# Kernel optimization log

Hardware: AMD Instinct MI355X
Metric: run time of the kernel (lower is better)

The kernel has to match this reference:

```python
import jax, jax.numpy as jnp
import numpy as np


def quantize_ternary(w):
    # BitNet b1.58: scale by mean |w|, round, clamp to {-1,0,1}
    gamma = jnp.maximum(jnp.mean(jnp.abs(w)), 1e-8)
    return jnp.clip(jnp.round(w / gamma), -1.0, 1.0)


def setup_inputs() -> dict:
    key = jax.random.key(0)
    k1, k2, k3 = jax.random.split(key, 3)
    in_features, out_features = 4096, 4096
    x = jax.random.normal(k1, (4, 2048, in_features), dtype=jnp.float32)
    # kaiming_uniform-like init
    bound_w = 1.0 / np.sqrt(in_features)
    weight = jax.random.uniform(k2, (out_features, in_features), dtype=jnp.float32,
                                minval=-bound_w * np.sqrt(3.0), maxval=bound_w * np.sqrt(3.0))
    bias = jax.random.uniform(k3, (out_features,), dtype=jnp.float32,
                              minval=-bound_w, maxval=bound_w)
    return {"x": x, "weight": weight, "bias": bias}


def reference(x, weight, bias):
    qw = quantize_ternary(weight)  # [out, in], values in {-1,0,1}
    # F.linear: x @ qw.T + bias
    return jnp.einsum('bsi,oi->bso', x, qw) + bias
```

## Files before the change

kernel.cpp:

```cpp
#include <hip/hip_runtime.h>
#include <stdint.h>

#define M_DIM 8192
#define N_DIM 4096
#define K_DIM 4096
#define BM 128
#define BN 128
#define BK 64

typedef int i32x4 __attribute__((ext_vector_type(4)));
typedef float f32x4 __attribute__((ext_vector_type(4)));

__device__ __forceinline__ void async_copy16(const void* g, void* l) {
    __builtin_amdgcn_global_load_lds(
        (const __attribute__((address_space(1))) void*)g,
        (__attribute__((address_space(3))) void*)l, 16, 0, 0);
}

__global__ __launch_bounds__(256) void abssum_partial(const float4* __restrict__ w,
                                                      double* __restrict__ partials) {
    const int lane = threadIdx.x & 63;
    const int wave = threadIdx.x >> 6;
    int base = blockIdx.x * 4096 + threadIdx.x;
    float s = 0.f;
    #pragma unroll
    for (int i = 0; i < 16; i++) {
        float4 v = w[base + i * 256];
        s += fabsf(v.x) + fabsf(v.y) + fabsf(v.z) + fabsf(v.w);
    }
    double d = (double)s;
    #pragma unroll
    for (int off = 32; off > 0; off >>= 1) d += __shfl_down(d, off, 64);
    __shared__ double wsum[4];
    if (lane == 0) wsum[wave] = d;
    __syncthreads();
    if (threadIdx.x == 0)
        partials[blockIdx.x] = (wsum[0] + wsum[1]) + (wsum[2] + wsum[3]);
}

__global__ __launch_bounds__(256) void gamma_reduce(const double* __restrict__ partials,
                                                    float* __restrict__ gamma_out) {
    const int lane = threadIdx.x & 63;
    const int wave = threadIdx.x >> 6;
    double d = partials[threadIdx.x] + partials[threadIdx.x + 256] +
               partials[threadIdx.x + 512] + partials[threadIdx.x + 768];
    #pragma unroll
    for (int off = 32; off > 0; off >>= 1) d += __shfl_down(d, off, 64);
    __shared__ double wsum[4];
    if (lane == 0) wsum[wave] = d;
    __syncthreads();
    if (threadIdx.x == 0) {
        double total = (wsum[0] + wsum[1]) + (wsum[2] + wsum[3]);
        float g = (float)(total * (1.0 / 16777216.0));
        gamma_out[0] = fmaxf(g, 1e-8f);
    }
}

__global__ __launch_bounds__(256) void wquant(const float4* __restrict__ w,
                                              char4* __restrict__ qw,
                                              const float* __restrict__ gamma_p, int n4) {
    float gamma = gamma_p[0];
    int i = blockIdx.x * blockDim.x + threadIdx.x;
    if (i >= n4) return;
    float4 v = w[i];
    char4 o;
    o.x = (signed char)fminf(fmaxf(rintf(v.x / gamma), -1.f), 1.f);
    o.y = (signed char)fminf(fmaxf(rintf(v.y / gamma), -1.f), 1.f);
    o.z = (signed char)fminf(fmaxf(rintf(v.z / gamma), -1.f), 1.f);
    o.w = (signed char)fminf(fmaxf(rintf(v.w / gamma), -1.f), 1.f);
    qw[i] = o;
}

__global__ __launch_bounds__(256) void xquant(const float* __restrict__ x,
                                              char* __restrict__ xq,
                                              float* __restrict__ xscale) {
    const int row = blockIdx.x;
    const int lane = threadIdx.x & 63;
    const int wave = threadIdx.x >> 6;
    const float4* xr = (const float4*)(x + (size_t)row * K_DIM);
    float m = 0.f;
    #pragma unroll
    for (int i = 0; i < 4; i++) {
        float4 v = xr[threadIdx.x + i * 256];
        m = fmaxf(m, fmaxf(fmaxf(fabsf(v.x), fabsf(v.y)), fmaxf(fabsf(v.z), fabsf(v.w))));
    }
    #pragma unroll
    for (int off = 32; off > 0; off >>= 1) m = fmaxf(m, __shfl_down(m, off, 64));
    __shared__ float wmax[4];
    if (lane == 0) wmax[wave] = m;
    __syncthreads();
    const float mx = fmaxf(fmaxf(wmax[0], wmax[1]), fmaxf(wmax[2], wmax[3]));
    const float scale = fmaxf(mx * (1.f / 127.f), 1e-30f);
    const float inv = 1.f / scale;
    if (threadIdx.x == 0) xscale[row] = scale;
    char4* oq = (char4*)(xq + (size_t)row * K_DIM);
    #pragma unroll
    for (int i = 0; i < 4; i++) {
        float4 v = xr[threadIdx.x + i * 256];
        char4 o;
        o.x = (signed char)fminf(fmaxf(rintf(v.x * inv), -127.f), 127.f);
        o.y = (signed char)fminf(fmaxf(rintf(v.y * inv), -127.f), 127.f);
        o.z = (signed char)fminf(fmaxf(rintf(v.z * inv), -127.f), 127.f);
        o.w = (signed char)fminf(fmaxf(rintf(v.w * inv), -127.f), 127.f);
        oq[threadIdx.x + i * 256] = o;
    }
}

__global__ __launch_bounds__(256) void gemm_kernel(
    const char* __restrict__ xq,
    const char* __restrict__ qw,
    const float* __restrict__ xscale,
    const float* __restrict__ bias,
    float* __restrict__ out)
{
    __shared__ __align__(16) char As[BM * BK];
    __shared__ __align__(16) char Bs[BN * BK];

    const int tid  = threadIdx.x;
    const int wave = tid >> 6;
    const int lane = tid & 63;
    const int wm   = (wave >> 1) * 64;
    const int wn   = (wave & 1) * 64;
    const int lm   = lane & 15;
    const int quad = lane >> 4;

    const int bm = blockIdx.y * BM;
    const int bn = blockIdx.x * BN;

    const int s0    = wave * 2;
    const int srow0 = s0 * 16 + (lane >> 2);
    const int srow1 = srow0 + 16;
    const int scol  = (lane & 3) * 16;

    const char* gA0 = xq + (size_t)(bm + srow0) * K_DIM + scol;
    const char* gA1 = xq + (size_t)(bm + srow1) * K_DIM + scol;
    const char* gB0 = qw + (size_t)(bn + srow0) * K_DIM + scol;
    const char* gB1 = qw + (size_t)(bn + srow1) * K_DIM + scol;

    char* lA0 = &As[(size_t)s0 * 1024];
    char* lA1 = &As[(size_t)(s0 + 1) * 1024];
    char* lB0 = &Bs[(size_t)s0 * 1024];
    char* lB1 = &Bs[(size_t)(s0 + 1) * 1024];

    i32x4 acc[4][4];
    #pragma unroll
    for (int i = 0; i < 4; i++)
        #pragma unroll
        for (int j = 0; j < 4; j++) acc[i][j] = (i32x4){0, 0, 0, 0};

    for (int kt = 0; kt < K_DIM; kt += BK) {
        async_copy16(gA0 + kt, lA0);
        async_copy16(gA1 + kt, lA1);
        async_copy16(gB0 + kt, lB0);
        async_copy16(gB1 + kt, lB1);
        __syncthreads();

        i32x4 a[4], b[4];
        #pragma unroll
        for (int mi = 0; mi < 4; mi++)
            a[mi] = *(const i32x4*)&As[(wm + mi * 16 + lm) * BK + quad * 16];
        #pragma unroll
        for (int ni = 0; ni < 4; ni++)
            b[ni] = *(const i32x4*)&Bs[(wn + ni * 16 + lm) * BK + quad * 16];

        #pragma unroll
        for (int mi = 0; mi < 4; mi++)
            #pragma unroll
            for (int ni = 0; ni < 4; ni++)
                acc[mi][ni] = __builtin_amdgcn_mfma_i32_16x16x64_i8(
                    a[mi], b[ni], acc[mi][ni], 0, 0, 0);

        __syncthreads();
    }

    float bl[4];
    #pragma unroll
    for (int ni = 0; ni < 4; ni++) bl[ni] = bias[bn + wn + ni * 16 + lm];

    #pragma unroll
    for (int mi = 0; mi < 4; mi++) {
        #pragma unroll
        for (int r = 0; r < 4; r++) {
            const int grow = bm + wm + mi * 16 + quad * 4 + r;
            const float sc = xscale[grow];
            float* orow = out + (size_t)grow * N_DIM + bn;
            #pragma unroll
            for (int ni = 0; ni < 4; ni++)
                orow[wn + ni * 16 + lm] = sc * (float)acc[mi][ni][r] + bl[ni];
        }
    }
}

extern "C" void kernel_launch(void* const* d_in, const int* in_sizes, int n_in,
                              void* d_out, int out_size, void* d_ws, size_t ws_size,
                              hipStream_t stream) {
    const float* x    = (const float*)d_in[0];
    const float* w    = (const float*)d_in[1];
    const float* bias = (const float*)d_in[2];
    float* out = (float*)d_out;

    char* ws = (char*)d_ws;
    char*   xq       = ws;
    char*   qw       = ws + (size_t)M_DIM * K_DIM;
    float*  xscale   = (float*)(qw + (size_t)N_DIM * K_DIM);
    double* partials = (double*)(xscale + M_DIM);
    float*  gamma_p  = (float*)(partials + 1024);

    const int wn4 = (N_DIM * K_DIM) / 4;

    abssum_partial<<<1024, 256, 0, stream>>>((const float4*)w, partials);
    gamma_reduce<<<1, 256, 0, stream>>>(partials, gamma_p);
    wquant<<<(wn4 + 255) / 256, 256, 0, stream>>>((const float4*)w, (char4*)qw, gamma_p, wn4);
    xquant<<<M_DIM, 256, 0, stream>>>(x, xq, xscale);

    dim3 grid(N_DIM / BN, M_DIM / BM);
    gemm_kernel<<<grid, 256, 0, stream>>>(xq, qw, xscale, bias, out);
}
```

Baseline: 428.9 us.

## Double GEMM K-tile to 128 with XOR-swizzled LDS layout and register-cached xquant

Doubles the GEMM K tile to 128 so each sync pair covers two MFMA k-steps, halving barrier and loop overhead per unit of work. The LDS layout gains an XOR swizzle on the 16-byte chunk index, applied in both the async global-to-LDS copy and the fragment reads, to reduce bank conflicts on the wider rows. xquant now keeps its loaded float4 values in registers instead of reading x from global memory twice. Shared memory per block doubles, which may lower occupancy.

```diff
diff --git a/kernel.cpp b/kernel.cpp
--- a/kernel.cpp
+++ b/kernel.cpp
@@ -6,10 +6,9 @@
 #define K_DIM 4096
 #define BM 128
 #define BN 128
-#define BK 64
+#define BK 128
 
 typedef int i32x4 __attribute__((ext_vector_type(4)));
-typedef float f32x4 __attribute__((ext_vector_type(4)));
 
 __device__ __forceinline__ void async_copy16(const void* g, void* l) {
     __builtin_amdgcn_global_load_lds(
@@ -71,18 +70,20 @@
     qw[i] = o;
 }
 
-__global__ __launch_bounds__(256) void xquant(const float* __restrict__ x,
-                                              char* __restrict__ xq,
+__global__ __launch_bounds__(256) void xquant(const float4* __restrict__ x,
+                                              char4* __restrict__ xq,
                                               float* __restrict__ xscale) {
     const int row = blockIdx.x;
     const int lane = threadIdx.x & 63;
     const int wave = threadIdx.x >> 6;
-    const float4* xr = (const float4*)(x + (size_t)row * K_DIM);
+    const float4* xr = x + (size_t)row * (K_DIM / 4);
+    float4 v[4];
     float m = 0.f;
     #pragma unroll
     for (int i = 0; i < 4; i++) {
-        float4 v = xr[threadIdx.x + i * 256];
-        m = fmaxf(m, fmaxf(fmaxf(fabsf(v.x), fabsf(v.y)), fmaxf(fabsf(v.z), fabsf(v.w))));
+        v[i] = xr[threadIdx.x + i * 256];
+        m = fmaxf(m, fmaxf(fmaxf(fabsf(v[i].x), fabsf(v[i].y)),
+                           fmaxf(fabsf(v[i].z), fabsf(v[i].w))));
     }
     #pragma unroll
     for (int off = 32; off > 0; off >>= 1) m = fmaxf(m, __shfl_down(m, off, 64));
@@ -93,15 +94,14 @@
     const float scale = fmaxf(mx * (1.f / 127.f), 1e-30f);
     const float inv = 1.f / scale;
     if (threadIdx.x == 0) xscale[row] = scale;
-    char4* oq = (char4*)(xq + (size_t)row * K_DIM);
+    char4* oq = xq + (size_t)row * (K_DIM / 4);
     #pragma unroll
     for (int i = 0; i < 4; i++) {
-        float4 v = xr[threadIdx.x + i * 256];
         char4 o;
-        o.x = (signed char)fminf(fmaxf(rintf(v.x * inv), -127.f), 127.f);
-        o.y = (signed char)fminf(fmaxf(rintf(v.y * inv), -127.f), 127.f);
-        o.z = (signed char)fminf(fmaxf(rintf(v.z * inv), -127.f), 127.f);
-        o.w = (signed char)fminf(fmaxf(rintf(v.w * inv), -127.f), 127.f);
+        o.x = (signed char)fminf(fmaxf(rintf(v[i].x * inv), -127.f), 127.f);
+        o.y = (signed char)fminf(fmaxf(rintf(v[i].y * inv), -127.f), 127.f);
+        o.z = (signed char)fminf(fmaxf(rintf(v[i].z * inv), -127.f), 127.f);
+        o.w = (signed char)fminf(fmaxf(rintf(v[i].w * inv), -127.f), 127.f);
         oq[threadIdx.x + i * 256] = o;
     }
 }
@@ -127,20 +127,18 @@
     const int bm = blockIdx.y * BM;
     const int bn = blockIdx.x * BN;
 
-    const int s0    = wave * 2;
-    const int srow0 = s0 * 16 + (lane >> 2);
-    const int srow1 = srow0 + 16;
-    const int scol  = (lane & 3) * 16;
-
-    const char* gA0 = xq + (size_t)(bm + srow0) * K_DIM + scol;
-    const char* gA1 = xq + (size_t)(bm + srow1) * K_DIM + scol;
-    const char* gB0 = qw + (size_t)(bn + srow0) * K_DIM + scol;
-    const char* gB1 = qw + (size_t)(bn + srow1) * K_DIM + scol;
-
-    char* lA0 = &As[(size_t)s0 * 1024];
-    char* lA1 = &As[(size_t)(s0 + 1) * 1024];
-    char* lB0 = &Bs[(size_t)s0 * 1024];
-    char* lB1 = &Bs[(size_t)(s0 + 1) * 1024];
+    const int sub = lane >> 3;
+    const int ch  = (lane & 7) ^ sub;
+    const int seg0 = wave * 4;
+
+    const char* gA[4];
+    const char* gB[4];
+    #pragma unroll
+    for (int i = 0; i < 4; i++) {
+        const int r = (seg0 + i) * 8 + sub;
+        gA[i] = xq + (size_t)(bm + r) * K_DIM + ch * 16;
+        gB[i] = qw + (size_t)(bn + r) * K_DIM + ch * 16;
+    }
 
     i32x4 acc[4][4];
     #pragma unroll
@@ -149,27 +147,31 @@
         for (int j = 0; j < 4; j++) acc[i][j] = (i32x4){0, 0, 0, 0};
 
     for (int kt = 0; kt < K_DIM; kt += BK) {
-        async_copy16(gA0 + kt, lA0);
-        async_copy16(gA1 + kt, lA1);
-        async_copy16(gB0 + kt, lB0);
-        async_copy16(gB1 + kt, lB1);
+        #pragma unroll
+        for (int i = 0; i < 4; i++) {
+            async_copy16(gA[i] + kt, &As[(seg0 + i) * 1024]);
+            async_copy16(gB[i] + kt, &Bs[(seg0 + i) * 1024]);
+        }
         __syncthreads();
 
-        i32x4 a[4], b[4];
-        #pragma unroll
-        for (int mi = 0; mi < 4; mi++)
-            a[mi] = *(const i32x4*)&As[(wm + mi * 16 + lm) * BK + quad * 16];
-        #pragma unroll
-        for (int ni = 0; ni < 4; ni++)
-            b[ni] = *(const i32x4*)&Bs[(wn + ni * 16 + lm) * BK + quad * 16];
-
-        #pragma unroll
-        for (int mi = 0; mi < 4; mi++)
+        #pragma unroll
+        for (int ks = 0; ks < 2; ks++) {
+            const int p = ((ks * 4 + quad) ^ (lm & 7)) * 16;
+            i32x4 a[4], b[4];
+            #pragma unroll
+            for (int mi = 0; mi < 4; mi++)
+                a[mi] = *(const i32x4*)&As[(wm + mi * 16 + lm) * BK + p];
             #pragma unroll
             for (int ni = 0; ni < 4; ni++)
-                acc[mi][ni] = __builtin_amdgcn_mfma_i32_16x16x64_i8(
-                    a[mi], b[ni], acc[mi][ni], 0, 0, 0);
-
+                b[ni] = *(const i32x4*)&Bs[(wn + ni * 16 + lm) * BK + p];
+
+            #pragma unroll
+            for (int mi = 0; mi < 4; mi++)
+                #pragma unroll
+                for (int ni = 0; ni < 4; ni++)
+                    acc[mi][ni] = __builtin_amdgcn_mfma_i32_16x16x64_i8(
+                        a[mi], b[ni], acc[mi][ni], 0, 0, 0);
+        }
         __syncthreads();
     }
 
@@ -211,7 +213,7 @@
     abssum_partial<<<1024, 256, 0, stream>>>((const float4*)w, partials);
     gamma_reduce<<<1, 256, 0, stream>>>(partials, gamma_p);
     wquant<<<(wn4 + 255) / 256, 256, 0, stream>>>((const float4*)w, (char4*)qw, gamma_p, wn4);
-    xquant<<<M_DIM, 256, 0, stream>>>(x, xq, xscale);
+    xquant<<<M_DIM, 256, 0, stream>>>((const float4*)x, (char4*)xq, xscale);
 
     dim3 grid(N_DIM / BN, M_DIM / BM);
     gemm_kernel<<<grid, 256, 0, stream>>>(xq, qw, xscale, bias, out);
```

After: 412.0 us. -3.9%, faster.
